# Kernel tuning notes

Hardware: AMD Instinct MI355X
Metric: run time of the kernel (lower is better)

## Reference

```python
import jax, jax.numpy as jnp
import numpy as np

B, S, E = 4, 1024, 1280
H = 16
D = E // H  # 80


def rotate_half(x):
    x1, x2 = jnp.split(x, 2, axis=-1)
    return jnp.concatenate([-x2, x1], axis=-1)


def setup_inputs() -> dict:
    key = jax.random.key(0)
    ks = jax.random.split(key, 12)
    sc = 0.02
    x = jax.random.normal(ks[0], (B, S, E), dtype=jnp.float32)
    # variable per-item sequence lengths (each <= S), cumulative
    lens = np.array([1024, 896, 768, 640], dtype=np.int32)
    cu_seqlens = jnp.asarray(np.concatenate([[0], np.cumsum(lens)]), dtype=jnp.int32)
    # rotary cos/sin for positions 0..S-1, head_dim D
    inv_freq = 1.0 / (10000.0 ** (np.arange(0, D, 2, dtype=np.float32) / D))
    t = np.arange(S, dtype=np.float32)
    freqs = np.outer(t, inv_freq)               # [S, D/2]
    emb = np.concatenate([freqs, freqs], axis=-1)  # [S, D]
    cos = jnp.asarray(np.cos(emb), dtype=jnp.float32)
    sin = jnp.asarray(np.sin(emb), dtype=jnp.float32)
    wq = jax.random.normal(ks[1], (E, E), dtype=jnp.float32) * sc
    bq = jax.random.normal(ks[2], (E,), dtype=jnp.float32) * sc
    wk = jax.random.normal(ks[3], (E, E), dtype=jnp.float32) * sc
    bk = jax.random.normal(ks[4], (E,), dtype=jnp.float32) * sc
    wv = jax.random.normal(ks[5], (E, E), dtype=jnp.float32) * sc
    bv = jax.random.normal(ks[6], (E,), dtype=jnp.float32) * sc
    wo = jax.random.normal(ks[7], (E, E), dtype=jnp.float32) * sc
    bo = jax.random.normal(ks[8], (E,), dtype=jnp.float32) * sc
    return {"x": x, "cu_seqlens": cu_seqlens, "cos": cos, "sin": sin,
            "wq": wq, "bq": bq, "wk": wk, "bk": bk, "wv": wv, "bv": bv,
            "wo": wo, "bo": bo}


def reference(x, cu_seqlens, cos, sin, wq, bq, wk, bk, wv, bv, wo, bo):
    b, s, e = x.shape
    h, d = H, D
    # QKV projections (nn.Linear: x @ W^T + b)
    q = (x @ wq.T + bq).reshape(b, s, h, d)
    k = (x @ wk.T + bk).reshape(b, s, h, d)
    v = (x @ wv.T + bv).reshape(b, s, h, d)
    # rotary embedding (apply_rotary_pos_emb, 'normal')
    c = cos[None, :, None, :]  # [1, s, 1, d]
    sn = sin[None, :, None, :]
    q = q * c + rotate_half(q) * sn
    k = k * c + rotate_half(k) * sn
    # patch attention mask from cu_seqlens (flatten_batch=False):
    # token i attends to token j iff i < len_b and j < len_b
    seq_lens = cu_seqlens[1:] - cu_seqlens[:-1]          # [b]
    idx = jnp.arange(s)
    valid = idx[None, :] < seq_lens[:, None]             # [b, s]
    mask = valid[:, None, :, None] & valid[:, None, None, :]  # [b, 1, s, s]
    # SDPA, non-causal
    scale = 1.0 / jnp.sqrt(jnp.asarray(d, dtype=q.dtype))
    scores = jnp.einsum("bqhd,bkhd->bhqk", q, k) * scale
    scores = jnp.where(mask, scores, jnp.asarray(-1e9, dtype=scores.dtype))
    attn = jax.nn.softmax(scores, axis=-1)
    out = jnp.einsum("bhqk,bkhd->bqhd", attn, v)         # [b, s, h, d]
    out = out.reshape(b, s, e)
    # output projection
    return out @ wo.T + bo
```

## Files before the change

kernel.cpp:

```cpp
#include <hip/hip_runtime.h>
#include <hip/hip_bf16.h>

#define B_ 4
#define S_ 1024
#define E_ 1280
#define H_ 16
#define D_ 80
#define M_ (B_*S_)
#define QBLK 128

typedef __hip_bfloat16 bf16;
using bf16x8 = __attribute__((ext_vector_type(8))) short;
using f32x4  = __attribute__((ext_vector_type(4))) float;

__device__ __forceinline__ float b2f(bf16 x){ return __bfloat162float(x); }
__device__ __forceinline__ bf16  f2b(float x){ return __float2bfloat16(x); }
__device__ __forceinline__ void  stf(float* p, float v){ *p = v; }
__device__ __forceinline__ void  stf(bf16*  p, float v){ *p = f2b(v); }

__device__ __forceinline__ void gload_lds16(const void* g, void* l) {
    __builtin_amdgcn_global_load_lds(
        (const __attribute__((address_space(1))) unsigned int*)g,
        (__attribute__((address_space(3))) unsigned int*)l, 16, 0, 0);
}

__device__ __forceinline__ void ph_begin() {
    __builtin_amdgcn_s_barrier();
    asm volatile("s_waitcnt lgkmcnt(0)" ::: "memory");
    __builtin_amdgcn_sched_barrier(0);
    __builtin_amdgcn_s_setprio(1);
}
__device__ __forceinline__ void ph_end() {
    __builtin_amdgcn_s_setprio(0);
    __builtin_amdgcn_sched_barrier(0);
    __builtin_amdgcn_s_barrier();
}
__device__ __forceinline__ void ph_end_vm6() {
    __builtin_amdgcn_s_setprio(0);
    __builtin_amdgcn_sched_barrier(0);
    asm volatile("s_waitcnt vmcnt(6)" ::: "memory");
    __builtin_amdgcn_s_barrier();
}
__device__ __forceinline__ void ph_end_vm0() {
    __builtin_amdgcn_s_setprio(0);
    __builtin_amdgcn_sched_barrier(0);
    asm volatile("s_waitcnt vmcnt(0)" ::: "memory");
    __builtin_amdgcn_s_barrier();
}

__global__ __launch_bounds__(256) void cvt_kernel(
    const float* __restrict__ s0, const float* __restrict__ s1,
    const float* __restrict__ s2, const float* __restrict__ s3,
    const float* __restrict__ s4,
    bf16* __restrict__ d0, bf16* __restrict__ d1, bf16* __restrict__ d2,
    bf16* __restrict__ d3, bf16* __restrict__ d4,
    int n0, int n1)
{
    const float* s; bf16* d; int n;
    switch (blockIdx.y) {
        case 0: s = s0; d = d0; n = n0; break;
        case 1: s = s1; d = d1; n = n1; break;
        case 2: s = s2; d = d2; n = n1; break;
        case 3: s = s3; d = d3; n = n1; break;
        default: s = s4; d = d4; n = n1; break;
    }
    int i = (blockIdx.x * 256 + threadIdx.x) * 8;
    if (i >= n) return;
    float4 a = *(const float4*)(s + i);
    float4 b = *(const float4*)(s + i + 4);
    bf16 t[8];
    t[0]=f2b(a.x); t[1]=f2b(a.y); t[2]=f2b(a.z); t[3]=f2b(a.w);
    t[4]=f2b(b.x); t[5]=f2b(b.y); t[6]=f2b(b.z); t[7]=f2b(b.w);
    *(uint4*)(d + i) = *(const uint4*)t;
}

__global__ __launch_bounds__(512, 2) void qkv_gemm_8ph(
    const bf16* __restrict__ A,
    const bf16* __restrict__ W0, const bf16* __restrict__ W1, const bf16* __restrict__ W2,
    const float* __restrict__ b0, const float* __restrict__ b1, const float* __restrict__ b2,
    bf16* __restrict__ Cq, bf16* __restrict__ Ck, bf16* __restrict__ Cv)
{
    constexpr int K = 1280;
    constexpr int NITER = K / 128;

    __shared__ __align__(16) bf16 Asm[2][2][128*64];
    __shared__ __align__(16) bf16 Bsm[2][2][128*64];

    const int bm  = blockIdx.x * 256;
    const int ny  = blockIdx.y;
    const int mat = ny / 5;
    const int bn  = (ny % 5) * 256;
    const bf16*  W    = (mat == 0) ? W0 : (mat == 1) ? W1 : W2;
    const float* bias = (mat == 0) ? b0 : (mat == 1) ? b1 : b2;

    const int tid  = threadIdx.x;
    const int lane = tid & 63, wv = tid >> 6;
    const int wm = wv >> 2, wn = wv & 3;
    const int quad = lane >> 4, l15 = lane & 15;

    auto stageA = [&](int j_, int half) {
        #pragma unroll
        for (int i = 0; i < 2; i++) {
            const int c   = tid + i*512;
            const int row = c >> 3;
            const int g   = (c & 7) ^ (row & 7);
            gload_lds16(A + (size_t)(bm + half*128 + row) * K + j_*64 + g*8,
                        &Asm[j_ & 1][half][(wv*64 + i*512) * 8]);
        }
    };
    auto stageB = [&](int j_, int half) {
        #pragma unroll
        for (int i = 0; i < 2; i++) {
            const int c   = tid + i*512;
            const int row = c >> 3;
            const int g   = (c & 7) ^ (row & 7);
            gload_lds16(W + (size_t)(bn + half*128 + row) * K + j_*64 + g*8,
                        &Bsm[j_ & 1][half][(wv*64 + i*512) * 8]);
        }
    };
    auto lda = [&](int bf, int mt, int ks) -> bf16x8 {
        const int r = mt*16 + l15;
        return *(const bf16x8*)&Asm[bf][wm][r*64 + (((quad + ks*4) ^ (r & 7)) << 3)];
    };
    auto ldb = [&](int bf, int nt, int ks) -> bf16x8 {
        const int r = (wn & 1)*64 + nt*16 + l15;
        return *(const bf16x8*)&Bsm[bf][wn >> 1][r*64 + (((quad + ks*4) ^ (r & 7)) << 3)];
    };

    f32x4 acc[8][4] = {};
    bf16x8 a[4][2], bA[2][2], bB[2][2];

#define MFMA_Q(MT0, NT0, BB_) do { \
    _Pragma("unroll") for (int mt_ = 0; mt_ < 4; mt_++) \
    _Pragma("unroll") for (int nt_ = 0; nt_ < 2; nt_++) \
    _Pragma("unroll") for (int ks_ = 0; ks_ < 2; ks_++) \
        acc[(MT0)+mt_][(NT0)+nt_] = __builtin_amdgcn_mfma_f32_16x16x32_bf16( \
            a[mt_][ks_], BB_[nt_][ks_], acc[(MT0)+mt_][(NT0)+nt_], 0, 0, 0); \
} while (0)

    stageA(0, 0); stageA(0, 1); stageB(0, 0); stageB(0, 1);
    stageA(1, 0); stageA(1, 1); stageB(1, 0); stageB(1, 1);
    __syncthreads();

    for (int t = 0; t < NITER; t++) {
        const int  j  = 2*t;
        const bool pf = (t + 1 < NITER);

        #pragma unroll
        for (int mt = 0; mt < 4; mt++) { a[mt][0] = lda(0, mt, 0); a[mt][1] = lda(0, mt, 1); }
        #pragma unroll
        for (int nt = 0; nt < 2; nt++) { bA[nt][0] = ldb(0, nt, 0); bA[nt][1] = ldb(0, nt, 1); }
        stageA(j+1, 1);
        ph_begin(); MFMA_Q(0, 0, bA); ph_end();

        #pragma unroll
        for (int nt = 0; nt < 2; nt++) { bB[nt][0] = ldb(0, 2+nt, 0); bB[nt][1] = ldb(0, 2+nt, 1); }
        ph_begin(); MFMA_Q(0, 2, bB); ph_end();

        #pragma unroll
        for (int mt = 0; mt < 4; mt++) { a[mt][0] = lda(0, 4+mt, 0); a[mt][1] = lda(0, 4+mt, 1); }
        if (pf) stageB(j+2, 0);
        ph_begin(); MFMA_Q(4, 0, bA); ph_end();

        if (pf) { stageB(j+2, 1); stageA(j+2, 0); }
        ph_begin(); MFMA_Q(4, 2, bB);
        if (pf) ph_end_vm6(); else ph_end_vm0();

        #pragma unroll
        for (int mt = 0; mt < 4; mt++) { a[mt][0] = lda(1, mt, 0); a[mt][1] = lda(1, mt, 1); }
        #pragma unroll
        for (int nt = 0; nt < 2; nt++) { bA[nt][0] = ldb(1, nt, 0); bA[nt][1] = ldb(1, nt, 1); }
        if (pf) stageA(j+2, 1);
        ph_begin(); MFMA_Q(0, 0, bA); ph_end();

        #pragma unroll
        for (int nt = 0; nt < 2; nt++) { bB[nt][0] = ldb(1, 2+nt, 0); bB[nt][1] = ldb(1, 2+nt, 1); }
        ph_begin(); MFMA_Q(0, 2, bB); ph_end();

        #pragma unroll
        for (int mt = 0; mt < 4; mt++) { a[mt][0] = lda(1, 4+mt, 0); a[mt][1] = lda(1, 4+mt, 1); }
        if (pf) stageB(j+3, 0);
        ph_begin(); MFMA_Q(4, 0, bA); ph_end();

        if (pf) { stageB(j+3, 1); stageA(j+3, 0); }
        ph_begin(); MFMA_Q(4, 2, bB); ph_end_vm6();
    }
#undef MFMA_Q

    if (mat < 2) {
        bf16* C = (mat == 0) ? Cq : Ck;
        #pragma unroll
        for (int nt = 0; nt < 4; nt++) {
            const int ncol = bn + wn*64 + nt*16 + l15;
            const float bv = bias[ncol];
            #pragma unroll
            for (int mt = 0; mt < 8; mt++) {
                const int m0 = bm + wm*128 + mt*16 + quad*4;
                #pragma unroll
                for (int r = 0; r < 4; r++)
                    C[(size_t)(m0 + r) * E_ + ncol] = f2b(acc[mt][nt][r] + bv);
            }
        }
    } else {
        #pragma unroll
        for (int nt = 0; nt < 4; nt++) {
            const int ncol = bn + wn*64 + nt*16 + l15;
            const float bv = bias[ncol];
            const int hh = ncol / 80, dd = ncol % 80;
            #pragma unroll
            for (int mt = 0; mt < 8; mt++) {
                const int m0  = bm + wm*128 + mt*16 + quad*4;
                const int btok = m0 >> 10;
                const int key  = m0 & 1023;
                union { bf16 h[4]; uint2 u; } t4;
                #pragma unroll
                for (int r = 0; r < 4; r++) t4.h[r] = f2b(acc[mt][nt][r] + bv);
                *(uint2*)&Cv[((size_t)(btok*H_ + hh)*D_ + dd)*S_ + key] = t4.u;
            }
        }
    }
}

template<typename TC, bool VT_OUT>
__global__ __launch_bounds__(256) void mfma_gemm_bt(
    const bf16* __restrict__ A,
    const bf16* __restrict__ W0, const bf16* __restrict__ W1, const bf16* __restrict__ W2,
    const float* __restrict__ b0, const float* __restrict__ b1, const float* __restrict__ b2,
    TC* __restrict__ C0, TC* __restrict__ C1, TC* __restrict__ C2,
    int K, int N, int ntiles)
{
    const int mat = blockIdx.y / ntiles;
    const int bn  = (blockIdx.y % ntiles) * 128;
    const int bm  = blockIdx.x * 128;
    const bf16* W; const float* bias; TC* C;
    if (mat == 0)      { W = W0; bias = b0; C = C0; }
    else if (mat == 1) { W = W1; bias = b1; C = C1; }
    else               { W = W2; bias = b2; C = C2; }

    __shared__ bf16 As[2][128][32];
    __shared__ bf16 Ws[2][128][32];

    const int tid  = threadIdx.x;
    const int lane = tid & 63;
    const int wv   = tid >> 6;
    const int wm   = (wv & 1) * 64;
    const int wn   = (wv >> 1) * 64;
    const int srow = wv * 16 + (lane >> 2);
    const int scol = (lane & 3) * 8;

    f32x4 acc[4][4] = {};

    for (int k0 = 0; k0 < K; k0 += 64) {
        __syncthreads();
        #pragma unroll
        for (int p = 0; p < 2; p++) {
            const int kc = k0 + p*32 + scol;
            gload_lds16(A + (size_t)(bm + srow)      * K + kc, &As[p][wv*16][0]);
            gload_lds16(A + (size_t)(bm + 64 + srow) * K + kc, &As[p][64 + wv*16][0]);
            gload_lds16(W + (size_t)(bn + srow)      * K + kc, &Ws[p][wv*16][0]);
            gload_lds16(W + (size_t)(bn + 64 + srow) * K + kc, &Ws[p][64 + wv*16][0]);
        }
        __syncthreads();

        const int fr = lane & 15;
        const int kq = (lane >> 4) * 8;
        #pragma unroll
        for (int p = 0; p < 2; p++) {
            bf16x8 af[4], wf[4];
            #pragma unroll
            for (int t = 0; t < 4; t++) {
                af[t] = *(const bf16x8*)&As[p][wm + t*16 + fr][kq];
                wf[t] = *(const bf16x8*)&Ws[p][wn + t*16 + fr][kq];
            }
            #pragma unroll
            for (int mt = 0; mt < 4; mt++)
                #pragma unroll
                for (int nt = 0; nt < 4; nt++)
                    acc[mt][nt] = __builtin_amdgcn_mfma_f32_16x16x32_bf16(
                        af[mt], wf[nt], acc[mt][nt], 0, 0, 0);
        }
    }

    const int col_l = lane & 15;
    const int row_l = (lane >> 4) * 4;

    if (VT_OUT && mat == 2) {
        const int btok = bm >> 10;
        const int keyb = (bm & 1023) + wm + row_l;
        #pragma unroll
        for (int nt = 0; nt < 4; nt++) {
            const int n = bn + wn + nt*16 + col_l;
            const float bv = bias[n];
            const int hh = n / 80, dd = n % 80;
            bf16* vbase = (bf16*)C + ((size_t)(btok*H_ + hh)*D_ + dd)*S_ + keyb;
            #pragma unroll
            for (int mt = 0; mt < 4; mt++) {
                union { bf16 h[4]; uint2 u; } t4;
                #pragma unroll
                for (int r = 0; r < 4; r++) t4.h[r] = f2b(acc[mt][nt][r] + bv);
                *(uint2*)&vbase[mt*16] = t4.u;
            }
        }
    } else {
        #pragma unroll
        for (int nt = 0; nt < 4; nt++) {
            const int n = bn + wn + nt*16 + col_l;
            const float bv = bias[n];
            #pragma unroll
            for (int mt = 0; mt < 4; mt++) {
                #pragma unroll
                for (int r = 0; r < 4; r++) {
                    const int m = bm + wm + mt*16 + row_l + r;
                    stf(&C[(size_t)m * N + n], acc[mt][nt][r] + bv);
                }
            }
        }
    }
}

__device__ __forceinline__ void rope8(const bf16* lo, const bf16* hi,
                                      const float* cp, const float* sp,
                                      float mul, uint4* out_lo, uint4* out_hi)
{
    union { uint4 u; bf16 h[8]; } li, hi_, lo_o, hi_o;
    li.u  = *(const uint4*)lo;
    hi_.u = *(const uint4*)hi;
    #pragma unroll
    for (int u = 0; u < 8; u++) {
        float x1 = b2f(li.h[u]), x2 = b2f(hi_.h[u]);
        float c = cp[u], s = sp[u];
        lo_o.h[u] = f2b((x1*c - x2*s) * mul);
        hi_o.h[u] = f2b((x2*c + x1*s) * mul);
    }
    *out_lo = lo_o.u;
    *out_hi = hi_o.u;
}

__global__ __launch_bounds__(256) void rope_kernel(
    bf16* __restrict__ qp, bf16* __restrict__ kp,
    const float* __restrict__ cosp, const float* __restrict__ sinp)
{
    int idx = blockIdx.x * 256 + threadIdx.x;
    const int NT = M_ * H_ * 5;
    bf16* base; float mul;
    if (idx < NT) { base = qp; mul = 0.11180339887498949f; }
    else         { base = kp; mul = 1.0f; idx -= NT; }
    const int row = idx / 80;
    const int rem = idx - row * 80;
    const int h   = rem / 5;
    const int pc  = rem - h * 5;
    const int s   = row & (S_ - 1);
    bf16* p = base + (size_t)row * E_ + h * D_ + pc * 8;
    const float* cp = cosp + s * D_ + pc * 8;
    const float* sp = sinp + s * D_ + pc * 8;
    uint4 olo, ohi;
    rope8(p, p + 40, cp, sp, mul, &olo, &ohi);
    *(uint4*)p        = olo;
    *(uint4*)(p + 40) = ohi;
}

__global__ __launch_bounds__(512, 4) void attn_mfma(
    const bf16* __restrict__ q, const bf16* __restrict__ k, const bf16* __restrict__ vt,
    const int* __restrict__ cu, bf16* __restrict__ o)
{
    __shared__ __align__(16) bf16 Ks[2][64*80];
    __shared__ __align__(16) bf16 VTs[2][80*64];
    __shared__ __align__(16) bf16 PTq[8][16*64];

    const int n  = blockIdx.x;
    const int g  = ((n >> 6) << 3) | (n & 7);
    const int qs = (n >> 3) & 7;
    const int b  = g >> 4;
    const int h  = g & 15;

    const int tid  = threadIdx.x;
    const int lane = tid & 63, wv = tid >> 6;
    const int quad = lane >> 4, l15 = lane & 15;
    const int q0   = qs * QBLK;
    const int len  = cu[b + 1] - cu[b];

    const bool uniformq = (q0 >= len);
    const bool clean    = ((len & (QBLK - 1)) == 0);
    const int  ktiles   = uniformq ? 16 : (clean ? (len >> 6) : 16);
    const bool domask   = !uniformq && !clean;

    bf16* PT = &PTq[wv][0];

    bf16x8 qf[3] = {};
    if (!uniformq) {
        const bf16* qrow = q + (size_t)(b*S_ + q0 + wv*16 + l15)*E_ + h*D_ + quad*8;
        qf[0] = *(const bf16x8*)(qrow);
        qf[1] = *(const bf16x8*)(qrow + 32);
        if (quad < 2) qf[2] = *(const bf16x8*)(qrow + 64);
    }

    float m_s = -1e30f, l_s = 0.f;
    f32x4 o_acc[5] = {};

    bf16x8 pone;
    {
        const short one_s = (short)0x3F80;
        #pragma unroll
        for (int i = 0; i < 8; i++) pone[i] = one_s;
    }

    const int u_  = l15 >> 2;
    const int s0r = quad ^ u_;
    const int sv0 = quad ^ (l15 & 7);

    auto stage = [&](int kt, int bf) {
        #pragma unroll
        for (int i = 0; i < 3; i++) {
            int c = tid + i * 512;
            if (c < 640) {
                if (!uniformq) {
                    int row = c / 10, s5 = c - row * 10;
                    int uu = (row >> 2) & 3;
                    int sg = (s5 < 8) ? (s5 ^ uu) : (8 + ((s5 ^ uu) & 1));
                    gload_lds16(k + (size_t)(b*S_ + kt*64 + row)*E_ + h*D_ + sg*8,
                                &Ks[bf][c*8]);
                }
            } else if (c < 1280) {
                int c2 = c - 640;
                int row = c2 >> 3, s5 = c2 & 7;
                int sg = s5 ^ (row & 7);
                gload_lds16(vt + ((size_t)(b*H_ + h)*D_ + row)*S_ + kt*64 + sg*8,
                            &VTs[bf][c2*8]);
            }
        }
    };

    stage(0, 0);
    __syncthreads();

    const bool q_full = (q0 + 64) <= len;

    for (int kt = 0; kt < ktiles; kt++) {
        const int cur = kt & 1;
        if (kt + 1 < ktiles) stage(kt + 1, cur ^ 1);

        bf16x8 pf0 = pone, pf1 = pone;
        if (!uniformq) {
            f32x4 s4[4];
            #pragma unroll
            for (int nt = 0; nt < 4; nt++) {
                const bf16* kr = &Ks[cur][(nt*16 + l15) * 80];
                bf16x8 kf0 = *(const bf16x8*)(kr + s0r*8);
                bf16x8 kf1 = *(const bf16x8*)(kr + 32 + s0r*8);
                bf16x8 kf2 = {};
                if (quad < 2) kf2 = *(const bf16x8*)(kr + 64 + (s0r & 1)*8);
                f32x4 a0 = {};
                a0 = __builtin_amdgcn_mfma_f32_16x16x32_bf16(kf0, qf[0], a0, 0, 0, 0);
                a0 = __builtin_amdgcn_mfma_f32_16x16x32_bf16(kf1, qf[1], a0, 0, 0, 0);
                a0 = __builtin_amdgcn_mfma_f32_16x16x32_bf16(kf2, qf[2], a0, 0, 0, 0);
                s4[nt] = a0;
            }

            float sv[4][4];
            if (!domask || (q_full && (kt*64 + 64) <= len)) {
                #pragma unroll
                for (int nt = 0; nt < 4; nt++)
                    #pragma unroll
                    for (int r = 0; r < 4; r++)
                        sv[nt][r] = s4[nt][r];
            } else {
                const bool vq = (q0 + wv*16 + l15) < len;
                #pragma unroll
                for (int nt = 0; nt < 4; nt++)
                    #pragma unroll
                    for (int r = 0; r < 4; r++) {
                        const bool vk = (kt*64 + nt*16 + quad*4 + r) < len;
                        sv[nt][r] = (vq && vk) ? s4[nt][r] : -1e9f;
                    }
            }

            float rm[4];
            #pragma unroll
            for (int nt = 0; nt < 4; nt++)
                rm[nt] = fmaxf(fmaxf(sv[nt][0], sv[nt][1]), fmaxf(sv[nt][2], sv[nt][3]));
            float sloc = fmaxf(fmaxf(rm[0], rm[1]), fmaxf(rm[2], rm[3]));
            sloc = fmaxf(sloc, __shfl_xor(sloc, 16, 64));
            sloc = fmaxf(sloc, __shfl_xor(sloc, 32, 64));
            const float mnew  = fmaxf(m_s, sloc);
            const float alpha = __expf(m_s - mnew);
            float p[4][4], lsum = 0.f;
            #pragma unroll
            for (int nt = 0; nt < 4; nt++)
                #pragma unroll
                for (int r = 0; r < 4; r++) {
                    p[nt][r] = __expf(sv[nt][r] - mnew);
                    lsum += p[nt][r];
                }
            lsum += __shfl_xor(lsum, 16, 64);
            lsum += __shfl_xor(lsum, 32, 64);
            l_s = l_s * alpha + lsum;
            m_s = mnew;
            #pragma unroll
            for (int dt = 0; dt < 5; dt++)
                #pragma unroll
                for (int r = 0; r < 4; r++)
                    o_acc[dt][r] *= alpha;

            #pragma unroll
            for (int nt = 0; nt < 4; nt++) {
                union { bf16 hh[4]; uint2 u; } w;
                #pragma unroll
                for (int r = 0; r < 4; r++) w.hh[r] = f2b(p[nt][r]);
                const int gw = (2*nt + (quad >> 1)) ^ (l15 & 7);
                *(uint2*)&PT[l15*64 + gw*8 + (quad & 1)*4] = w.u;
            }
            pf0 = *(const bf16x8*)&PT[l15*64 + ((quad    ) ^ (l15 & 7))*8];
            pf1 = *(const bf16x8*)&PT[l15*64 + ((quad + 4) ^ (l15 & 7))*8];
        }

        #pragma unroll
        for (int dt = 0; dt < 5; dt++) {
            const bf16* vr = &VTs[cur][(dt*16 + l15) * 64];
            bf16x8 vf0 = *(const bf16x8*)(vr + sv0*8);
            bf16x8 vf1 = *(const bf16x8*)(vr + (sv0 ^ 4)*8);
            o_acc[dt] = __builtin_amdgcn_mfma_f32_16x16x32_bf16(vf0, pf0, o_acc[dt], 0, 0, 0);
            o_acc[dt] = __builtin_amdgcn_mfma_f32_16x16x32_bf16(vf1, pf1, o_acc[dt], 0, 0, 0);
        }
        __syncthreads();
    }

    const float inv = uniformq ? (1.0f / 1024.0f) : (1.0f / l_s);
    const size_t row_g = (size_t)(b*S_ + q0 + wv*16 + l15);
    #pragma unroll
    for (int dt = 0; dt < 5; dt++) {
        union { bf16 hh[4]; uint2 u; } t4;
        #pragma unroll
        for (int r = 0; r < 4; r++) t4.hh[r] = f2b(o_acc[dt][r] * inv);
        *(uint2*)&o[row_g*E_ + h*D_ + dt*16 + quad*4] = t4.u;
    }
}

extern "C" void kernel_launch(void* const* d_in, const int* in_sizes, int n_in,
                              void* d_out, int out_size, void* d_ws, size_t ws_size,
                              hipStream_t stream)
{
    const float* x    = (const float*)d_in[0];
    const int*   cu   = (const int*)  d_in[1];
    const float* cosp = (const float*)d_in[2];
    const float* sinp = (const float*)d_in[3];
    const float* wq   = (const float*)d_in[4];
    const float* bq   = (const float*)d_in[5];
    const float* wk   = (const float*)d_in[6];
    const float* bk   = (const float*)d_in[7];
    const float* wv   = (const float*)d_in[8];
    const float* bv   = (const float*)d_in[9];
    const float* wo   = (const float*)d_in[10];
    const float* bo   = (const float*)d_in[11];
    float* out = (float*)d_out;

    bf16* q   = (bf16*)d_ws;
    bf16* kk  = q   + (size_t)M_ * E_;
    bf16* vt  = kk  + (size_t)M_ * E_;
    bf16* ao  = vt  + (size_t)M_ * E_;
    bf16* xb  = ao  + (size_t)M_ * E_;
    bf16* wqb = xb  + (size_t)M_ * E_;
    bf16* wkb = wqb + (size_t)E_ * E_;
    bf16* wvb = wkb + (size_t)E_ * E_;
    bf16* wob = wvb + (size_t)E_ * E_;

    cvt_kernel<<<dim3(2560, 5), 256, 0, stream>>>(
        x, wq, wk, wv, wo, xb, wqb, wkb, wvb, wob, M_*E_, E_*E_);

    qkv_gemm_8ph<<<dim3(M_/256, 15), 512, 0, stream>>>(
        xb, wqb, wkb, wvb, bq, bk, bv, q, kk, vt);

    rope_kernel<<<2560, 256, 0, stream>>>(q, kk, cosp, sinp);

    attn_mfma<<<512, 512, 0, stream>>>(q, kk, vt, cu, ao);

    mfma_gemm_bt<float, false><<<dim3(M_/128, 10), 256, 0, stream>>>(
        ao, wob, wob, wob, bo, bo, bo, out, out, out, E_, E_, 10);
}
```

Measured before the change: 230.8 us.

## Double query rows per attention warp and remap QKV GEMM block order

The attention kernel now handles 256 query rows per block, with each warp processing two 16-row query tiles. Each K/V tile staged in shared memory is therefore reused for twice as many queries, and the kernel launches half as many blocks. The QKV GEMM block index is remapped so that groups of 8 consecutive blocks are spread across different output tiles, likely to improve XCD/L2 locality. In exchange, registers per thread roughly double (launch bounds drop the occupancy hint), fewer blocks may underfill the GPU, and the masking fast path is now coarser.

```diff
diff --git a/kernel.cpp b/kernel.cpp
--- a/kernel.cpp
+++ b/kernel.cpp
@@ -7,7 +7,6 @@
 #define H_ 16
 #define D_ 80
 #define M_ (B_*S_)
-#define QBLK 128
 
 typedef __hip_bfloat16 bf16;
 using bf16x8 = __attribute__((ext_vector_type(8))) short;
@@ -86,8 +85,10 @@
     __shared__ __align__(16) bf16 Asm[2][2][128*64];
     __shared__ __align__(16) bf16 Bsm[2][2][128*64];
 
-    const int bm  = blockIdx.x * 256;
-    const int ny  = blockIdx.y;
+    const int flat = blockIdx.y * 16 + blockIdx.x;
+    const int nw   = (flat & 7) * 30 + (flat >> 3);
+    const int bm  = (nw & 15) * 256;
+    const int ny  = nw >> 4;
     const int mat = ny / 5;
     const int bn  = (ny % 5) * 256;
     const bf16*  W    = (mat == 0) ? W0 : (mat == 1) ? W1 : W2;
@@ -359,43 +360,48 @@
     *(uint4*)(p + 40) = ohi;
 }
 
-__global__ __launch_bounds__(512, 4) void attn_mfma(
+__global__ __launch_bounds__(512) void attn_mfma(
     const bf16* __restrict__ q, const bf16* __restrict__ k, const bf16* __restrict__ vt,
     const int* __restrict__ cu, bf16* __restrict__ o)
 {
     __shared__ __align__(16) bf16 Ks[2][64*80];
     __shared__ __align__(16) bf16 VTs[2][80*64];
-    __shared__ __align__(16) bf16 PTq[8][16*64];
+    __shared__ __align__(16) bf16 PTq[8][2][16*64];
 
     const int n  = blockIdx.x;
-    const int g  = ((n >> 6) << 3) | (n & 7);
-    const int qs = (n >> 3) & 7;
+    const int g  = ((n >> 5) << 3) | (n & 7);
+    const int qs = (n >> 3) & 3;
     const int b  = g >> 4;
     const int h  = g & 15;
 
     const int tid  = threadIdx.x;
     const int lane = tid & 63, wv = tid >> 6;
     const int quad = lane >> 4, l15 = lane & 15;
-    const int q0   = qs * QBLK;
+    const int q0   = qs * 256;
     const int len  = cu[b + 1] - cu[b];
 
     const bool uniformq = (q0 >= len);
-    const bool clean    = ((len & (QBLK - 1)) == 0);
-    const int  ktiles   = uniformq ? 16 : (clean ? (len >> 6) : 16);
-    const bool domask   = !uniformq && !clean;
-
-    bf16* PT = &PTq[wv][0];
-
-    bf16x8 qf[3] = {};
+    const bool fast     = !uniformq && ((q0 + 256) <= len) && ((len & 63) == 0);
+    const int  ktiles   = uniformq ? 16 : (fast ? (len >> 6) : 16);
+    const bool domask   = !uniformq && !fast;
+
+    bf16* PTa = &PTq[wv][0][0];
+    bf16* PTb = &PTq[wv][1][0];
+
+    bf16x8 qfA[3] = {}, qfB[3] = {};
     if (!uniformq) {
-        const bf16* qrow = q + (size_t)(b*S_ + q0 + wv*16 + l15)*E_ + h*D_ + quad*8;
-        qf[0] = *(const bf16x8*)(qrow);
-        qf[1] = *(const bf16x8*)(qrow + 32);
-        if (quad < 2) qf[2] = *(const bf16x8*)(qrow + 64);
-    }
-
-    float m_s = -1e30f, l_s = 0.f;
-    f32x4 o_acc[5] = {};
+        const bf16* qra = q + (size_t)(b*S_ + q0 + wv*32 + l15)*E_ + h*D_ + quad*8;
+        qfA[0] = *(const bf16x8*)(qra);
+        qfA[1] = *(const bf16x8*)(qra + 32);
+        if (quad < 2) qfA[2] = *(const bf16x8*)(qra + 64);
+        const bf16* qrb = qra + (size_t)16 * E_;
+        qfB[0] = *(const bf16x8*)(qrb);
+        qfB[1] = *(const bf16x8*)(qrb + 32);
+        if (quad < 2) qfB[2] = *(const bf16x8*)(qrb + 64);
+    }
+
+    float mA = -1e30f, lA = 0.f, mB = -1e30f, lB = 0.f;
+    f32x4 oA[5] = {}, oB[5] = {};
 
     bf16x8 pone;
     {
@@ -433,15 +439,67 @@
     stage(0, 0);
     __syncthreads();
 
-    const bool q_full = (q0 + 64) <= len;
+    auto softmax_pt = [&](f32x4* s4, float& m_s, float& l_s, f32x4* oc,
+                          bf16* PTg, bool vq, int kt) {
+        float sv[4][4];
+        if (!domask) {
+            #pragma unroll
+            for (int nt = 0; nt < 4; nt++)
+                #pragma unroll
+                for (int r = 0; r < 4; r++)
+                    sv[nt][r] = s4[nt][r];
+        } else {
+            #pragma unroll
+            for (int nt = 0; nt < 4; nt++)
+                #pragma unroll
+                for (int r = 0; r < 4; r++) {
+                    const bool vk = (kt*64 + nt*16 + quad*4 + r) < len;
+                    sv[nt][r] = (vq && vk) ? s4[nt][r] : -1e9f;
+                }
+        }
+        float rm[4];
+        #pragma unroll
+        for (int nt = 0; nt < 4; nt++)
+            rm[nt] = fmaxf(fmaxf(sv[nt][0], sv[nt][1]), fmaxf(sv[nt][2], sv[nt][3]));
+        float sloc = fmaxf(fmaxf(rm[0], rm[1]), fmaxf(rm[2], rm[3]));
+        sloc = fmaxf(sloc, __shfl_xor(sloc, 16, 64));
+        sloc = fmaxf(sloc, __shfl_xor(sloc, 32, 64));
+        const float mnew  = fmaxf(m_s, sloc);
+        const float alpha = __expf(m_s - mnew);
+        float p[4][4], lsum = 0.f;
+        #pragma unroll
+        for (int nt = 0; nt < 4; nt++)
+            #pragma unroll
+            for (int r = 0; r < 4; r++) {
+                p[nt][r] = __expf(sv[nt][r] - mnew);
+                lsum += p[nt][r];
+            }
+        lsum += __shfl_xor(lsum, 16, 64);
+        lsum += __shfl_xor(lsum, 32, 64);
+        l_s = l_s * alpha + lsum;
+        m_s = mnew;
+        #pragma unroll
+        for (int dt = 0; dt < 5; dt++)
+            #pragma unroll
+            for (int r = 0; r < 4; r++)
+                oc[dt][r] *= alpha;
+        #pragma unroll
+        for (int nt = 0; nt < 4; nt++) {
+            union { bf16 hh[4]; uint2 u; } w;
+            #pragma unroll
+            for (int r = 0; r < 4; r++) w.hh[r] = f2b(p[nt][r]);
+            const int gw = (2*nt + (quad >> 1)) ^ (l15 & 7);
+            *(uint2*)&PTg[l15*64 + gw*8 + (quad & 1)*4] = w.u;
+        }
+    };
 
     for (int kt = 0; kt < ktiles; kt++) {
         const int cur = kt & 1;
         if (kt + 1 < ktiles) stage(kt + 1, cur ^ 1);
 
-        bf16x8 pf0 = pone, pf1 = pone;
+        bf16x8 pfA0 = pone, pfA1 = pone, pfB0 = pone, pfB1 = pone;
         if (!uniformq) {
-            f32x4 s4[4];
+            f32x4 sa[4], sb[4];
             #pragma unroll
             for (int nt = 0; nt < 4; nt++) {
                 const bf16* kr = &Ks[cur][(nt*16 + l15) * 80];
@@ -449,68 +507,25 @@
                 bf16x8 kf1 = *(const bf16x8*)(kr + 32 + s0r*8);
                 bf16x8 kf2 = {};
                 if (quad < 2) kf2 = *(const bf16x8*)(kr + 64 + (s0r & 1)*8);
-                f32x4 a0 = {};
-                a0 = __builtin_amdgcn_mfma_f32_16x16x32_bf16(kf0, qf[0], a0, 0, 0, 0);
-                a0 = __builtin_amdgcn_mfma_f32_16x16x32_bf16(kf1, qf[1], a0, 0, 0, 0);
-                a0 = __builtin_amdgcn_mfma_f32_16x16x32_bf16(kf2, qf[2], a0, 0, 0, 0);
-                s4[nt] = a0;
-            }
-
-            float sv[4][4];
-            if (!domask || (q_full && (kt*64 + 64) <= len)) {
-                #pragma unroll
-                for (int nt = 0; nt < 4; nt++)
-                    #pragma unroll
-                    for (int r = 0; r < 4; r++)
-                        sv[nt][r] = s4[nt][r];
-            } else {
-                const bool vq = (q0 + wv*16 + l15) < len;
-                #pragma unroll
-                for (int nt = 0; nt < 4; nt++)
-                    #pragma unroll
-                    for (int r = 0; r < 4; r++) {
-                        const bool vk = (kt*64 + nt*16 + quad*4 + r) < len;
-                        sv[nt][r] = (vq && vk) ? s4[nt][r] : -1e9f;
-                    }
-            }
-
-            float rm[4];
-            #pragma unroll
-            for (int nt = 0; nt < 4; nt++)
-                rm[nt] = fmaxf(fmaxf(sv[nt][0], sv[nt][1]), fmaxf(sv[nt][2], sv[nt][3]));
-            float sloc = fmaxf(fmaxf(rm[0], rm[1]), fmaxf(rm[2], rm[3]));
-            sloc = fmaxf(sloc, __shfl_xor(sloc, 16, 64));
-            sloc = fmaxf(sloc, __shfl_xor(sloc, 32, 64));
-            const float mnew  = fmaxf(m_s, sloc);
-            const float alpha = __expf(m_s - mnew);
-            float p[4][4], lsum = 0.f;
-            #pragma unroll
-            for (int nt = 0; nt < 4; nt++)
-                #pragma unroll
-                for (int r = 0; r < 4; r++) {
-                    p[nt][r] = __expf(sv[nt][r] - mnew);
-                    lsum += p[nt][r];
-                }
-            lsum += __shfl_xor(lsum, 16, 64);
-            lsum += __shfl_xor(lsum, 32, 64);
-            l_s = l_s * alpha + lsum;
-            m_s = mnew;
-            #pragma unroll
-            for (int dt = 0; dt < 5; dt++)
-                #pragma unroll
-                for (int r = 0; r < 4; r++)
-                    o_acc[dt][r] *= alpha;
-
-            #pragma unroll
-            for (int nt = 0; nt < 4; nt++) {
-                union { bf16 hh[4]; uint2 u; } w;
-                #pragma unroll
-                for (int r = 0; r < 4; r++) w.hh[r] = f2b(p[nt][r]);
-                const int gw = (2*nt + (quad >> 1)) ^ (l15 & 7);
-                *(uint2*)&PT[l15*64 + gw*8 + (quad & 1)*4] = w.u;
-            }
-            pf0 = *(const bf16x8*)&PT[l15*64 + ((quad    ) ^ (l15 & 7))*8];
-            pf1 = *(const bf16x8*)&PT[l15*64 + ((quad + 4) ^ (l15 & 7))*8];
+                f32x4 a0 = {}, b0 = {};
+                a0 = __builtin_amdgcn_mfma_f32_16x16x32_bf16(kf0, qfA[0], a0, 0, 0, 0);
+                a0 = __builtin_amdgcn_mfma_f32_16x16x32_bf16(kf1, qfA[1], a0, 0, 0, 0);
+                a0 = __builtin_amdgcn_mfma_f32_16x16x32_bf16(kf2, qfA[2], a0, 0, 0, 0);
+                b0 = __builtin_amdgcn_mfma_f32_16x16x32_bf16(kf0, qfB[0], b0, 0, 0, 0);
+                b0 = __builtin_amdgcn_mfma_f32_16x16x32_bf16(kf1, qfB[1], b0, 0, 0, 0);
+                b0 = __builtin_amdgcn_mfma_f32_16x16x32_bf16(kf2, qfB[2], b0, 0, 0, 0);
+                sa[nt] = a0; sb[nt] = b0;
+            }
+
+            const bool vqA = (q0 + wv*32 + l15) < len;
+            const bool vqB = (q0 + wv*32 + 16 + l15) < len;
+            softmax_pt(sa, mA, lA, oA, PTa, vqA, kt);
+            softmax_pt(sb, mB, lB, oB, PTb, vqB, kt);
+
+            pfA0 = *(const bf16x8*)&PTa[l15*64 + ((quad    ) ^ (l15 & 7))*8];
+            pfA1 = *(const bf16x8*)&PTa[l15*64 + ((quad + 4) ^ (l15 & 7))*8];
+            pfB0 = *(const bf16x8*)&PTb[l15*64 + ((quad    ) ^ (l15 & 7))*8];
+            pfB1 = *(const bf16x8*)&PTb[l15*64 + ((quad + 4) ^ (l15 & 7))*8];
         }
 
         #pragma unroll
@@ -518,20 +533,33 @@
             const bf16* vr = &VTs[cur][(dt*16 + l15) * 64];
             bf16x8 vf0 = *(const bf16x8*)(vr + sv0*8);
             bf16x8 vf1 = *(const bf16x8*)(vr + (sv0 ^ 4)*8);
-            o_acc[dt] = __builtin_amdgcn_mfma_f32_16x16x32_bf16(vf0, pf0, o_acc[dt], 0, 0, 0);
-            o_acc[dt] = __builtin_amdgcn_mfma_f32_16x16x32_bf16(vf1, pf1, o_acc[dt], 0, 0, 0);
+            oA[dt] = __builtin_amdgcn_mfma_f32_16x16x32_bf16(vf0, pfA0, oA[dt], 0, 0, 0);
+            oA[dt] = __builtin_amdgcn_mfma_f32_16x16x32_bf16(vf1, pfA1, oA[dt], 0, 0, 0);
+            oB[dt] = __builtin_amdgcn_mfma_f32_16x16x32_bf16(vf0, pfB0, oB[dt], 0, 0, 0);
+            oB[dt] = __builtin_amdgcn_mfma_f32_16x16x32_bf16(vf1, pfB1, oB[dt], 0, 0, 0);
         }
         __syncthreads();
     }
 
-    const float inv = uniformq ? (1.0f / 1024.0f) : (1.0f / l_s);
-    const size_t row_g = (size_t)(b*S_ + q0 + wv*16 + l15);
-    #pragma unroll
-    for (int dt = 0; dt < 5; dt++) {
-        union { bf16 hh[4]; uint2 u; } t4;
-        #pragma unroll
-        for (int r = 0; r < 4; r++) t4.hh[r] = f2b(o_acc[dt][r] * inv);
-        *(uint2*)&o[row_g*E_ + h*D_ + dt*16 + quad*4] = t4.u;
+    {
+        const float invA = uniformq ? (1.0f / 1024.0f) : (1.0f / lA);
+        const size_t ra = (size_t)(b*S_ + q0 + wv*32 + l15);
+        #pragma unroll
+        for (int dt = 0; dt < 5; dt++) {
+            union { bf16 hh[4]; uint2 u; } t4;
+            #pragma unroll
+            for (int r = 0; r < 4; r++) t4.hh[r] = f2b(oA[dt][r] * invA);
+            *(uint2*)&o[ra*E_ + h*D_ + dt*16 + quad*4] = t4.u;
+        }
+        const float invB = uniformq ? (1.0f / 1024.0f) : (1.0f / lB);
+        const size_t rb = ra + 16;
+        #pragma unroll
+        for (int dt = 0; dt < 5; dt++) {
+            union { bf16 hh[4]; uint2 u; } t4;
+            #pragma unroll
+            for (int r = 0; r < 4; r++) t4.hh[r] = f2b(oB[dt][r] * invB);
+            *(uint2*)&o[rb*E_ + h*D_ + dt*16 + quad*4] = t4.u;
+        }
     }
 }
 
@@ -566,12 +594,12 @@
     cvt_kernel<<<dim3(2560, 5), 256, 0, stream>>>(
         x, wq, wk, wv, wo, xb, wqb, wkb, wvb, wob, M_*E_, E_*E_);
 
-    qkv_gemm_8ph<<<dim3(M_/256, 15), 512, 0, stream>>>(
+    qkv_gemm_8ph<<<dim3(16, 15), 512, 0, stream>>>(
         xb, wqb, wkb, wvb, bq, bk, bv, q, kk, vt);
 
     rope_kernel<<<2560, 256, 0, stream>>>(q, kk, cosp, sinp);
 
-    attn_mfma<<<512, 512, 0, stream>>>(q, kk, vt, cu, ao);
+    attn_mfma<<<256, 512, 0, stream>>>(q, kk, vt, cu, ao);
 
     mfma_gemm_bt<float, false><<<dim3(M_/128, 10), 256, 0, stream>>>(
         ao, wob, wob, wob, bo, bo, bo, out, out, out, E_, E_, 10);
```

Measured after the change: 243.3 us. 5.4% more time.
